# Optimization experiments

Measured on AMD Instinct MI355X. Metric: run time of the kernel, lower is better.

Reference implementation:

```python
import jax, jax.numpy as jnp
import numpy as np
import math

B, H, N, D = 4, 16, 2048, 64
EPS = 1e-8


def setup_inputs() -> dict:
    key = jax.random.key(0)
    kq, kk, kv = jax.random.split(key, 3)
    Q = jax.random.normal(kq, (B, H, N, D), dtype=jnp.float32)
    K = jax.random.normal(kk, (B, H, N, D), dtype=jnp.float32)
    V = jax.random.normal(kv, (B, H, N, D), dtype=jnp.float32)
    # learnable per-head scale, init g0 = log2(N^2 - N)
    g0 = math.log2(N * N - N)
    qk_scale = jnp.full((H,), g0, dtype=jnp.float32)
    # causal mask, broadcast over (B, H)
    M = jnp.tril(jnp.ones((N, N), dtype=bool))
    return {"Q": Q, "K": K, "V": V, "qk_scale": qk_scale, "M": M}


def reference(Q, K, V, qk_scale, M):
    # L2-normalize Q and K along head dim (cosine attention)
    Q_hat = Q / (jnp.sqrt(jnp.sum(Q * Q, axis=-1, keepdims=True)) + EPS)
    K_hat = K / (jnp.sqrt(jnp.sum(K * K, axis=-1, keepdims=True)) + EPS)
    g = qk_scale[None, :, None, None]  # per-head learnable temperature
    scores = jnp.einsum('bhnd,bhmd->bhnm', Q_hat * g, K_hat)
    scores = jnp.where(M, scores, -jnp.inf)
    attn = jax.nn.softmax(scores, axis=-1)  # stable max-subtract softmax
    return jnp.einsum('bhnm,bhmd->bhnd', attn, V)
```

## Files before the change

kernel.cpp:

```cpp
#include <hip/hip_runtime.h>


#define BATCH 4
#define HEADS 16
#define SEQ   2048
#define DIM   64
#define EPS   1e-8f
#define LOG2E 1.44269504088896340736f

typedef short bf16x8 __attribute__((ext_vector_type(8)));
typedef short s16x4  __attribute__((ext_vector_type(4)));
typedef float fx16   __attribute__((ext_vector_type(16)));
typedef unsigned int u32x4 __attribute__((ext_vector_type(4)));

static __device__ __forceinline__ short f2bf(float x) {
    unsigned u = __float_as_uint(x);
    unsigned r = (u + 0x7fffu + ((u >> 16) & 1u)) >> 16;
    return (short)r;
}
static __device__ __forceinline__ unsigned cvt_pk(float lo, float hi) {
    unsigned r;
    asm("v_cvt_pk_bf16_f32 %0, %1, %2" : "=v"(r) : "v"(lo), "v"(hi));
    return r;
}
static __device__ __forceinline__ void gload_lds16(const short* g, short* l) {
    __builtin_amdgcn_global_load_lds(
        (const __attribute__((address_space(1))) void*)g,
        (__attribute__((address_space(3))) void*)l, 16, 0, 0);
}

__global__ __launch_bounds__(256) void norm_k(
    const float* __restrict__ K, short* __restrict__ Kn)
{
    const int tid  = threadIdx.x;
    const int lane = tid & 63;
    long long rid = (long long)blockIdx.x * 16 + (tid >> 6) * 4 + (lane >> 4);
    const int c4 = (lane & 15) * 4;

    const float* src = K + rid * DIM;
    float4 v = *(const float4*)(src + c4);
    float ss = v.x * v.x + v.y * v.y + v.z * v.z + v.w * v.w;
    ss += __shfl_xor(ss, 1);
    ss += __shfl_xor(ss, 2);
    ss += __shfl_xor(ss, 4);
    ss += __shfl_xor(ss, 8);
    float s = 1.0f / (sqrtf(ss) + EPS);

    const int bh = (int)(rid >> 11);
    const int n  = (int)(rid & 2047);
    const int kt = n >> 6;
    const int r  = n & 63;
    short* dst = Kn + ((size_t)bh << 17) + (kt << 12) + (r << 6);

    s16x4 o;
    o[0] = f2bf(v.x * s);
    o[1] = f2bf(v.y * s);
    o[2] = f2bf(v.z * s);
    o[3] = f2bf(v.w * s);
    *(s16x4*)(dst + (c4 ^ ((r & 7) << 3))) = o;
}

#define TLDS 68

__global__ __launch_bounds__(256) void transpose_v(
    const float* __restrict__ V, short* __restrict__ Vt)
{
    const int nt = blockIdx.x;
    const int bh = blockIdx.y;
    const float* Vb = V + ((size_t)bh * SEQ + (size_t)nt * 64) * DIM;
    short* Vo = Vt + ((size_t)bh << 17) + (nt << 12);

    __shared__ short lds[DIM * TLDS];
    const int t  = threadIdx.x;
    const int cg = t & 15;
    const int rr = t >> 4;

#pragma unroll
    for (int i = 0; i < 4; ++i) {
        int n  = rr + i * 16;
        int d0 = cg * 4;
        float4 v = *(const float4*)(Vb + (size_t)n * DIM + d0);
        lds[(d0 + 0) * TLDS + n] = f2bf(v.x);
        lds[(d0 + 1) * TLDS + n] = f2bf(v.y);
        lds[(d0 + 2) * TLDS + n] = f2bf(v.z);
        lds[(d0 + 3) * TLDS + n] = f2bf(v.w);
    }
    __syncthreads();
#pragma unroll
    for (int i = 0; i < 4; ++i) {
        int d  = rr + i * 16;
        int nl = cg * 4;
        s16x4 o;
        o[0] = lds[d * TLDS + nl + 0];
        o[1] = lds[d * TLDS + nl + 1];
        o[2] = lds[d * TLDS + nl + 2];
        o[3] = lds[d * TLDS + nl + 3];
        *(s16x4*)(Vo + (d << 6) + (nl ^ ((d & 7) << 3))) = o;
    }
}

__global__ __launch_bounds__(512) void attn_fwd(
    const float* __restrict__ Q, const float* __restrict__ scale,
    const short* __restrict__ Kn, const short* __restrict__ Vt,
    float* __restrict__ out)
{
    const int lid = blockIdx.x;
    const int bh  = (lid & 7) * 8 + ((lid >> 3) & 7);
    const int qb  = 7 - (lid >> 6);
    const int tid = threadIdx.x;
    const int w   = tid >> 6;
    const int l   = tid & 63;
    const int lq  = l & 31;
    const int hi  = l >> 5;

    const short* Kb = Kn + ((size_t)bh << 17);
    const short* Vb = Vt + ((size_t)bh << 17);
    const float  g  = scale[bh & (HEADS - 1)];

    __shared__ __align__(16) short ldsK[3][64 * 64];
    __shared__ __align__(16) short ldsV[3][64 * 64];

    const int toff = tid * 8;

    const int wlo  = qb * 256 + w * 32;
    const int whi  = wlo + 31;
    const int qrow = wlo + lq;
    const int nkt  = 4 * qb + 4;

    gload_lds16(Kb + toff,        &ldsK[0][toff]);
    gload_lds16(Vb + toff,        &ldsV[0][toff]);
    gload_lds16(Kb + 4096 + toff, &ldsK[1][toff]);
    gload_lds16(Vb + 4096 + toff, &ldsV[1][toff]);

    const float* Qrow = Q + ((size_t)bh * SEQ + qrow) * DIM;
    float qv[4][8];
    float ss = 0.f;
#pragma unroll
    for (int c = 0; c < 4; ++c) {
        float4 a = *(const float4*)(Qrow + c * 16 + hi * 8);
        float4 b = *(const float4*)(Qrow + c * 16 + hi * 8 + 4);
        qv[c][0] = a.x; qv[c][1] = a.y; qv[c][2] = a.z; qv[c][3] = a.w;
        qv[c][4] = b.x; qv[c][5] = b.y; qv[c][6] = b.z; qv[c][7] = b.w;
#pragma unroll
        for (int jj = 0; jj < 8; ++jj) ss += qv[c][jj] * qv[c][jj];
    }
    ss += __shfl_xor(ss, 32);
    const float sc = g * LOG2E / (sqrtf(ss) + EPS);

    bf16x8 qbf[4];
#pragma unroll
    for (int c = 0; c < 4; ++c) {
        u32x4 wds;
#pragma unroll
        for (int m = 0; m < 4; ++m)
            wds[m] = cvt_pk(qv[c][2 * m] * sc, qv[c][2 * m + 1] * sc);
        qbf[c] = __builtin_bit_cast(bf16x8, wds);
    }

    fx16 oacc[2];
#pragma unroll
    for (int dt = 0; dt < 2; ++dt)
#pragma unroll
        for (int r = 0; r < 16; ++r) oacc[dt][r] = 0.f;
    float lsum = 0.f;

    int cur = 0;
    for (int kt = 0; kt < nkt; ++kt) {
        __builtin_amdgcn_s_barrier();

        if (kt + 2 < nkt) {
            int nb = cur + 2; if (nb >= 3) nb -= 3;
            const short* gK = Kb + (size_t)(kt + 2) * 4096;
            const short* gV = Vb + (size_t)(kt + 2) * 4096;
            gload_lds16(gK + toff, &ldsK[nb][toff]);
            gload_lds16(gV + toff, &ldsV[nb][toff]);
            asm volatile("s_waitcnt vmcnt(4)" ::: "memory");
        } else if (kt + 1 < nkt) {
            asm volatile("s_waitcnt vmcnt(2)" ::: "memory");
        } else {
            asm volatile("s_waitcnt vmcnt(0)" ::: "memory");
        }
        __builtin_amdgcn_s_barrier();

        const int k0 = kt * 64;
        if (k0 <= whi) {
            const short* lk = ldsK[cur];
            const short* lv = ldsV[cur];

            fx16 sacc[2];
#pragma unroll
            for (int t = 0; t < 2; ++t)
#pragma unroll
                for (int r = 0; r < 16; ++r) sacc[t][r] = 0.f;

            bf16x8 kf[2][4];
#pragma unroll
            for (int t = 0; t < 2; ++t)
#pragma unroll
                for (int c = 0; c < 4; ++c) {
                    int r = t * 32 + lq;
                    kf[t][c] = *(const bf16x8*)
                        &lk[(r << 6) + ((c * 16 + hi * 8) ^ ((r & 7) << 3))];
                }
            __builtin_amdgcn_s_setprio(1);
#pragma unroll
            for (int c = 0; c < 4; ++c) {
                sacc[0] = __builtin_amdgcn_mfma_f32_32x32x16_bf16(kf[0][c], qbf[c], sacc[0], 0, 0, 0);
                sacc[1] = __builtin_amdgcn_mfma_f32_32x32x16_bf16(kf[1][c], qbf[c], sacc[1], 0, 0, 0);
            }
            __builtin_amdgcn_s_setprio(0);

            bf16x8 vf[2][4];
#pragma unroll
            for (int dt = 0; dt < 2; ++dt)
#pragma unroll
                for (int ks = 0; ks < 4; ++ks) {
                    int d = dt * 32 + lq;
                    vf[dt][ks] = *(const bf16x8*)
                        &lv[(d << 6) + ((ks * 16 + hi * 8) ^ ((d & 7) << 3))];
                }

            float pv[32];
#pragma unroll
            for (int t = 0; t < 2; ++t)
#pragma unroll
                for (int r = 0; r < 16; ++r) pv[t * 16 + r] = sacc[t][r];

            if (k0 + 63 > wlo) {
#pragma unroll
                for (int t = 0; t < 2; ++t)
#pragma unroll
                    for (int r = 0; r < 16; ++r) {
                        int key = k0 + 32 * t + (r & 3) + 8 * (r >> 2) + 4 * hi;
                        if (key > qrow) pv[t * 16 + r] = -3.0e38f;
                    }
            }

#pragma unroll
            for (int r = 0; r < 32; ++r)
                pv[r] = __builtin_amdgcn_exp2f(pv[r]);

            float ts[16];
#pragma unroll
            for (int r = 0; r < 16; ++r) ts[r] = pv[r] + pv[r + 16];
#pragma unroll
            for (int r = 0; r < 8; ++r) ts[r] += ts[r + 8];
#pragma unroll
            for (int r = 0; r < 4; ++r) ts[r] += ts[r + 4];
            float ps = (ts[0] + ts[1]) + (ts[2] + ts[3]);
            ps += __shfl_xor(ps, 32);
            lsum += ps;

            u32x4 paw[4];
#pragma unroll
            for (int ks = 0; ks < 4; ++ks) {
                const int t = ks >> 1;
                const int b0 = (ks & 1) * 8;
#pragma unroll
                for (int m = 0; m < 2; ++m) {
                    unsigned a = cvt_pk(pv[t * 16 + b0 + 2 * m], pv[t * 16 + b0 + 2 * m + 1]);
                    unsigned b = cvt_pk(pv[t * 16 + b0 + 2 * m + 4], pv[t * 16 + b0 + 2 * m + 5]);
                    asm("v_permlane32_swap_b32 %0, %1" : "+v"(a), "+v"(b));
                    paw[ks][m]     = a;
                    paw[ks][m + 2] = b;
                }
            }

            __builtin_amdgcn_s_setprio(1);
#pragma unroll
            for (int dt = 0; dt < 2; ++dt)
#pragma unroll
                for (int ks = 0; ks < 4; ++ks) {
                    bf16x8 pa = __builtin_bit_cast(bf16x8, paw[ks]);
                    oacc[dt] = __builtin_amdgcn_mfma_f32_32x32x16_bf16(vf[dt][ks], pa, oacc[dt], 0, 0, 0);
                }
            __builtin_amdgcn_s_setprio(0);
        }
        cur = (cur == 2) ? 0 : cur + 1;
    }

    float inv = 1.0f / lsum;
    size_t rb = ((size_t)bh * SEQ + (size_t)qrow) * DIM;
#pragma unroll
    for (int dt = 0; dt < 2; ++dt)
#pragma unroll
        for (int g4 = 0; g4 < 4; ++g4) {
            float4 o4;
            o4.x = oacc[dt][4 * g4 + 0] * inv;
            o4.y = oacc[dt][4 * g4 + 1] * inv;
            o4.z = oacc[dt][4 * g4 + 2] * inv;
            o4.w = oacc[dt][4 * g4 + 3] * inv;
            *(float4*)(out + rb + dt * 32 + 8 * g4 + 4 * hi) = o4;
        }
}

extern "C" void kernel_launch(void* const* d_in, const int* in_sizes, int n_in,
                              void* d_out, int out_size, void* d_ws, size_t ws_size,
                              hipStream_t stream)
{
    const float* Q  = (const float*)d_in[0];
    const float* K  = (const float*)d_in[1];
    const float* V  = (const float*)d_in[2];
    const float* qs = (const float*)d_in[3];
    float* out = (float*)d_out;

    const size_t nElem = (size_t)BATCH * HEADS * SEQ * DIM;
    short* Kn = (short*)d_ws;
    short* Vt = Kn + nElem;

    {
        long long rows = (long long)BATCH * HEADS * SEQ;
        norm_k<<<(int)(rows / 16), 256, 0, stream>>>(K, Kn);
    }
    {
        dim3 grid(SEQ / 64, BATCH * HEADS);
        transpose_v<<<grid, 256, 0, stream>>>(V, Vt);
    }
    {
        attn_fwd<<<(SEQ / 256) * BATCH * HEADS, 512, 0, stream>>>(Q, qs, Kn, Vt, out);
    }
}
```

Measured before the change: 73.90 us.

## Double-buffer 128-row KV stages and pair heavy/light query blocks in grid order

The K/V pipeline moves from a triple-buffered 64-row schedule to a double-buffered 128-row schedule. Each stage now processes two 64-key sub-tiles between barriers, which halves the barrier and waitcnt count per key. The block-to-query-tile mapping also changes so that the second half of the grid runs query blocks in ascending order, which aims to balance causal workload across waves. The Q loads are now issued before the first K/V prefetch. In exchange, prefetch depth drops to one stage ahead, and LDS use rises slightly.

```diff
diff --git a/kernel.cpp b/kernel.cpp
--- a/kernel.cpp
+++ b/kernel.cpp
@@ -105,8 +105,9 @@
     float* __restrict__ out)
 {
     const int lid = blockIdx.x;
+    const int q2  = lid >> 6;
+    const int qb  = (lid < 256) ? (7 - q2) : (q2 - 4);
     const int bh  = (lid & 7) * 8 + ((lid >> 3) & 7);
-    const int qb  = 7 - (lid >> 6);
     const int tid = threadIdx.x;
     const int w   = tid >> 6;
     const int l   = tid & 63;
@@ -117,33 +118,36 @@
     const short* Vb = Vt + ((size_t)bh << 17);
     const float  g  = scale[bh & (HEADS - 1)];
 
-    __shared__ __align__(16) short ldsK[3][64 * 64];
-    __shared__ __align__(16) short ldsV[3][64 * 64];
+    __shared__ __align__(16) short ldsK[2][128 * 64];
+    __shared__ __align__(16) short ldsV[2][128 * 64];
 
     const int toff = tid * 8;
 
     const int wlo  = qb * 256 + w * 32;
     const int whi  = wlo + 31;
     const int qrow = wlo + lq;
-    const int nkt  = 4 * qb + 4;
-
-    gload_lds16(Kb + toff,        &ldsK[0][toff]);
-    gload_lds16(Vb + toff,        &ldsV[0][toff]);
-    gload_lds16(Kb + 4096 + toff, &ldsK[1][toff]);
-    gload_lds16(Vb + 4096 + toff, &ldsV[1][toff]);
+    const int nr   = 2 * qb + 2;
 
     const float* Qrow = Q + ((size_t)bh * SEQ + qrow) * DIM;
     float qv[4][8];
-    float ss = 0.f;
 #pragma unroll
     for (int c = 0; c < 4; ++c) {
         float4 a = *(const float4*)(Qrow + c * 16 + hi * 8);
         float4 b = *(const float4*)(Qrow + c * 16 + hi * 8 + 4);
         qv[c][0] = a.x; qv[c][1] = a.y; qv[c][2] = a.z; qv[c][3] = a.w;
         qv[c][4] = b.x; qv[c][5] = b.y; qv[c][6] = b.z; qv[c][7] = b.w;
+    }
+
+    gload_lds16(Kb + toff,        &ldsK[0][toff]);
+    gload_lds16(Kb + 4096 + toff, &ldsK[0][4096 + toff]);
+    gload_lds16(Vb + toff,        &ldsV[0][toff]);
+    gload_lds16(Vb + 4096 + toff, &ldsV[0][4096 + toff]);
+
+    float ss = 0.f;
+#pragma unroll
+    for (int c = 0; c < 4; ++c)
 #pragma unroll
         for (int jj = 0; jj < 8; ++jj) ss += qv[c][jj] * qv[c][jj];
-    }
     ss += __shfl_xor(ss, 32);
     const float sc = g * LOG2E / (sqrtf(ss) + EPS);
 
@@ -165,27 +169,29 @@
     float lsum = 0.f;
 
     int cur = 0;
-    for (int kt = 0; kt < nkt; ++kt) {
+    for (int rr = 0; rr < nr; ++rr) {
         __builtin_amdgcn_s_barrier();
 
-        if (kt + 2 < nkt) {
-            int nb = cur + 2; if (nb >= 3) nb -= 3;
-            const short* gK = Kb + (size_t)(kt + 2) * 4096;
-            const short* gV = Vb + (size_t)(kt + 2) * 4096;
-            gload_lds16(gK + toff, &ldsK[nb][toff]);
-            gload_lds16(gV + toff, &ldsV[nb][toff]);
+        if (rr + 1 < nr) {
+            const int nb = cur ^ 1;
+            const short* gK = Kb + (size_t)(rr + 1) * 8192;
+            const short* gV = Vb + (size_t)(rr + 1) * 8192;
+            gload_lds16(gK + toff,        &ldsK[nb][toff]);
+            gload_lds16(gK + 4096 + toff, &ldsK[nb][4096 + toff]);
+            gload_lds16(gV + toff,        &ldsV[nb][toff]);
+            gload_lds16(gV + 4096 + toff, &ldsV[nb][4096 + toff]);
             asm volatile("s_waitcnt vmcnt(4)" ::: "memory");
-        } else if (kt + 1 < nkt) {
-            asm volatile("s_waitcnt vmcnt(2)" ::: "memory");
         } else {
             asm volatile("s_waitcnt vmcnt(0)" ::: "memory");
         }
         __builtin_amdgcn_s_barrier();
 
-        const int k0 = kt * 64;
-        if (k0 <= whi) {
-            const short* lk = ldsK[cur];
-            const short* lv = ldsV[cur];
+#pragma unroll
+        for (int s = 0; s < 2; ++s) {
+            const int k0 = rr * 128 + s * 64;
+            if (k0 > whi) continue;
+            const short* lk = &ldsK[cur][s * 4096];
+            const short* lv = &ldsV[cur][s * 4096];
 
             fx16 sacc[2];
 #pragma unroll
@@ -276,7 +282,7 @@
                 }
             __builtin_amdgcn_s_setprio(0);
         }
-        cur = (cur == 2) ? 0 : cur + 1;
+        cur ^= 1;
     }
 
     float inv = 1.0f / lsum;
```

Measured after the change: 76.14 us. +3.0%, slower.

## Fuse K-normalize and V-transpose prep kernels and reorder attention block schedule

Applied to the files above, without the earlier changes.

Merges the K normalization kernel and the V transpose kernel into a single prep kernel, removing one launch and its tail. Changes the causal block ordering so the first half of the grid runs heavy-to-light query blocks and the second half runs light-to-heavy, pairing work for better load balance. Moves the Q global loads ahead of the K/V LDS prefetch issue. The block-order change alters which blocks run concurrently and could shift the tail behaviour.

```diff
diff --git a/kernel.cpp b/kernel.cpp
--- a/kernel.cpp
+++ b/kernel.cpp
@@ -29,52 +29,42 @@
         (__attribute__((address_space(3))) void*)l, 16, 0, 0);
 }
 
-__global__ __launch_bounds__(256) void norm_k(
-    const float* __restrict__ K, short* __restrict__ Kn)
-{
-    const int tid  = threadIdx.x;
-    const int lane = tid & 63;
-    long long rid = (long long)blockIdx.x * 16 + (tid >> 6) * 4 + (lane >> 4);
-    const int c4 = (lane & 15) * 4;
-
-    const float* src = K + rid * DIM;
-    float4 v = *(const float4*)(src + c4);
-    float ss = v.x * v.x + v.y * v.y + v.z * v.z + v.w * v.w;
-    ss += __shfl_xor(ss, 1);
-    ss += __shfl_xor(ss, 2);
-    ss += __shfl_xor(ss, 4);
-    ss += __shfl_xor(ss, 8);
-    float s = 1.0f / (sqrtf(ss) + EPS);
-
-    const int bh = (int)(rid >> 11);
-    const int n  = (int)(rid & 2047);
-    const int kt = n >> 6;
-    const int r  = n & 63;
-    short* dst = Kn + ((size_t)bh << 17) + (kt << 12) + (r << 6);
-
-    s16x4 o;
-    o[0] = f2bf(v.x * s);
-    o[1] = f2bf(v.y * s);
-    o[2] = f2bf(v.z * s);
-    o[3] = f2bf(v.w * s);
-    *(s16x4*)(dst + (c4 ^ ((r & 7) << 3))) = o;
-}
-
 #define TLDS 68
 
-__global__ __launch_bounds__(256) void transpose_v(
-    const float* __restrict__ V, short* __restrict__ Vt)
+__global__ __launch_bounds__(256) void prep_kv(
+    const float* __restrict__ K, const float* __restrict__ V,
+    short* __restrict__ Kn, short* __restrict__ Vt)
 {
     const int nt = blockIdx.x;
     const int bh = blockIdx.y;
+    const int tid = threadIdx.x;
+
+    const float* Kb = K + ((size_t)bh * SEQ + (size_t)nt * 64) * DIM;
+    short* Kno = Kn + ((size_t)bh << 17) + (nt << 12);
+    const int c4 = (tid & 15) * 4;
+#pragma unroll
+    for (int i = 0; i < 4; ++i) {
+        const int r = i * 16 + (tid >> 4);
+        float4 v = *(const float4*)(Kb + (size_t)r * DIM + c4);
+        float ss = v.x * v.x + v.y * v.y + v.z * v.z + v.w * v.w;
+        ss += __shfl_xor(ss, 1);
+        ss += __shfl_xor(ss, 2);
+        ss += __shfl_xor(ss, 4);
+        ss += __shfl_xor(ss, 8);
+        float s = 1.0f / (sqrtf(ss) + EPS);
+        s16x4 o;
+        o[0] = f2bf(v.x * s);
+        o[1] = f2bf(v.y * s);
+        o[2] = f2bf(v.z * s);
+        o[3] = f2bf(v.w * s);
+        *(s16x4*)(Kno + (r << 6) + (c4 ^ ((r & 7) << 3))) = o;
+    }
+
     const float* Vb = V + ((size_t)bh * SEQ + (size_t)nt * 64) * DIM;
     short* Vo = Vt + ((size_t)bh << 17) + (nt << 12);
-
     __shared__ short lds[DIM * TLDS];
-    const int t  = threadIdx.x;
-    const int cg = t & 15;
-    const int rr = t >> 4;
-
+    const int cg = tid & 15;
+    const int rr = tid >> 4;
 #pragma unroll
     for (int i = 0; i < 4; ++i) {
         int n  = rr + i * 16;
@@ -105,8 +95,9 @@
     float* __restrict__ out)
 {
     const int lid = blockIdx.x;
+    const int q2  = lid >> 6;
+    const int qb  = (lid < 256) ? (7 - q2) : (q2 - 4);
     const int bh  = (lid & 7) * 8 + ((lid >> 3) & 7);
-    const int qb  = 7 - (lid >> 6);
     const int tid = threadIdx.x;
     const int w   = tid >> 6;
     const int l   = tid & 63;
@@ -127,23 +118,26 @@
     const int qrow = wlo + lq;
     const int nkt  = 4 * qb + 4;
 
-    gload_lds16(Kb + toff,        &ldsK[0][toff]);
-    gload_lds16(Vb + toff,        &ldsV[0][toff]);
-    gload_lds16(Kb + 4096 + toff, &ldsK[1][toff]);
-    gload_lds16(Vb + 4096 + toff, &ldsV[1][toff]);
-
     const float* Qrow = Q + ((size_t)bh * SEQ + qrow) * DIM;
     float qv[4][8];
-    float ss = 0.f;
 #pragma unroll
     for (int c = 0; c < 4; ++c) {
         float4 a = *(const float4*)(Qrow + c * 16 + hi * 8);
         float4 b = *(const float4*)(Qrow + c * 16 + hi * 8 + 4);
         qv[c][0] = a.x; qv[c][1] = a.y; qv[c][2] = a.z; qv[c][3] = a.w;
         qv[c][4] = b.x; qv[c][5] = b.y; qv[c][6] = b.z; qv[c][7] = b.w;
+    }
+
+    gload_lds16(Kb + toff,        &ldsK[0][toff]);
+    gload_lds16(Vb + toff,        &ldsV[0][toff]);
+    gload_lds16(Kb + 4096 + toff, &ldsK[1][toff]);
+    gload_lds16(Vb + 4096 + toff, &ldsV[1][toff]);
+
+    float ss = 0.f;
+#pragma unroll
+    for (int c = 0; c < 4; ++c)
 #pragma unroll
         for (int jj = 0; jj < 8; ++jj) ss += qv[c][jj] * qv[c][jj];
-    }
     ss += __shfl_xor(ss, 32);
     const float sc = g * LOG2E / (sqrtf(ss) + EPS);
 
@@ -309,12 +303,8 @@
     short* Vt = Kn + nElem;
 
     {
-        long long rows = (long long)BATCH * HEADS * SEQ;
-        norm_k<<<(int)(rows / 16), 256, 0, stream>>>(K, Kn);
-    }
-    {
         dim3 grid(SEQ / 64, BATCH * HEADS);
-        transpose_v<<<grid, 256, 0, stream>>>(V, Vt);
+        prep_kv<<<grid, 256, 0, stream>>>(K, V, Kn, Vt);
     }
     {
         attn_fwd<<<(SEQ / 256) * BATCH * HEADS, 512, 0, stream>>>(Q, qs, Kn, Vt, out);
```

Result: slower. 78.51 us (+6.2%).
